# Performance work log

Measured on AMD Instinct MI355X. Metric: run time of the kernel, lower is better.

The kernel has to match this reference:

```python
import jax, jax.numpy as jnp
import numpy as np
import math

S, B, H, NH = 2048, 2, 2048, 16
HN = H // NH  # head dim = 128

def setup_inputs() -> dict:
    key = jax.random.key(0)
    ks = jax.random.split(key, 5)
    hidden_states = jax.random.normal(ks[0], (S, B, H), dtype=jnp.float32)
    # causal mask: True means masked (filled with -10000), broadcast over heads
    attention_mask = jnp.triu(jnp.ones((S, S), dtype=bool), k=1)[None, None].repeat(B, axis=0)
    w_qkv = jax.random.normal(ks[1], (3 * H, H), dtype=jnp.float32) * (1.0 / math.sqrt(H))
    b_qkv = jax.random.normal(ks[2], (3 * H,), dtype=jnp.float32) * 0.02
    w_dense = jax.random.normal(ks[3], (H, H), dtype=jnp.float32) * (1.0 / math.sqrt(H))
    b_dense = jax.random.normal(ks[4], (H,), dtype=jnp.float32) * 0.02
    return {"hidden_states": hidden_states, "attention_mask": attention_mask,
            "w_qkv": w_qkv, "b_qkv": b_qkv, "w_dense": w_dense, "b_dense": b_dense}

def reference(hidden_states, attention_mask, w_qkv, b_qkv, w_dense, b_dense):
    s, b, h = hidden_states.shape
    nh, hn = NH, h // NH
    # QKV projection (ColumnParallelLinear, world_size=1)
    qkv = hidden_states @ w_qkv.T + b_qkv                # [s, b, 3h]
    qkv = qkv.reshape(s, b, nh, 3 * hn)
    q, k, v = jnp.split(qkv, 3, axis=-1)                 # each [s, b, nh, hn]
    q = q.transpose(1, 2, 0, 3)                          # [b, nh, s, hn]
    k = k.transpose(1, 2, 0, 3)
    v = v.transpose(1, 2, 0, 3)
    # norm_factor = sqrt(hn)*coeff, softmax rescales by coeff -> net 1/sqrt(hn)
    scores = jnp.einsum('bnqh,bnkh->bnqk', q, k) / jnp.float32(math.sqrt(hn))
    scores = jnp.where(attention_mask, jnp.float32(-10000.0), scores)
    probs = jax.nn.softmax(scores, axis=-1)              # [b, nh, s, s]
    ctx = jnp.einsum('bnqk,bnkh->bnqh', probs, v)        # [b, nh, s, hn]
    ctx = ctx.transpose(2, 0, 1, 3).reshape(s, b, h)     # [s, b, h]
    # RowParallelLinear with skip_bias_add=True: bias returned separately
    output = ctx @ w_dense.T
    return output, b_dense
```

## Files before the change

kernel.cpp:

```cpp
#include <hip/hip_runtime.h>

typedef unsigned short u16;
typedef unsigned int   u32;
typedef __attribute__((ext_vector_type(8))) short bf16x8;
typedef __attribute__((ext_vector_type(4))) float f32x4;

#define S_LEN 2048
#define B_SZ  2
#define H_DIM 2048
#define NH_   16
#define HN_   128
#define M_TOK 4096
#define NQKV  6144
#define NT_   (S_LEN / 64)

#define BAR      asm volatile("s_barrier" ::: "memory")
#define WAITV(n) asm volatile("s_waitcnt vmcnt(" #n ")" ::: "memory")

__device__ __forceinline__ u16 f2bf(float f) {
    u32 x = __float_as_uint(f);
    return (u16)((x + 0x7fffu + ((x >> 16) & 1u)) >> 16);
}

__device__ __forceinline__ void async16(const void* g, void* l) {
    __builtin_amdgcn_global_load_lds((const __attribute__((address_space(1))) void*)g,
                                     (__attribute__((address_space(3))) void*)l,
                                     16, 0, 0);
}

__global__ __launch_bounds__(256) void cvt3(
    const float* __restrict__ a, u16* __restrict__ oa, int na,
    const float* __restrict__ b, u16* __restrict__ ob, int nb,
    const float* __restrict__ c, u16* __restrict__ oc, int nc)
{
    int g = blockIdx.x * 256 + threadIdx.x;
    const float* in; u16* out; int idx;
    if (g < na)           { in = a; out = oa; idx = g; }
    else if (g < na + nb) { in = b; out = ob; idx = g - na; }
    else if (g < na + nb + nc) { in = c; out = oc; idx = g - na - nb; }
    else return;
    int i = idx * 4;
    float4 v = *(const float4*)&in[i];
    ushort4 o;
    o.x = f2bf(v.x); o.y = f2bf(v.y); o.z = f2bf(v.z); o.w = f2bf(v.w);
    *(ushort4*)&out[i] = o;
}

template<int EPI, int MM, int NN>
__global__ __launch_bounds__(512, 2) void gemm8(
    const u16* __restrict__ A, const u16* __restrict__ W,
    const float* __restrict__ bias, float* __restrict__ Cout,
    u16* __restrict__ Qb, u16* __restrict__ Kb, u16* __restrict__ Vt)
{
    constexpr int K   = 2048;
    constexpr int NKT = K / 64;
    constexpr int NBN = NN / 256;
    constexpr int NWG = (MM / 256) * NBN;

    __shared__ __align__(16) u16 sA[2][256 * 64];
    __shared__ __align__(16) u16 sB[2][256 * 64];

    const int t = threadIdx.x, l = t & 63, w = t >> 6;
    const int quad = l >> 4, ln = l & 15;
    const int qw_r = w >> 2, qw_c = w & 3;

    int wg = blockIdx.x;
    wg = (wg & 7) * (NWG / 8) + (wg >> 3);
    const int m0 = (wg / NBN) * 256, n0 = (wg % NBN) * 256;

    const int srow = t >> 3;
    const int skc  = (t & 7) ^ (srow & 7);
    const u16* pA = A + (size_t)(m0 + srow) * K + skc * 8;
    const u16* pB = W + (size_t)(n0 + srow) * K + skc * 8;

#define STAGE_A(db, h, kt)                                                        \
    do {                                                                          \
        async16(pA + (size_t)(h) * 128 * K + (size_t)(kt) * 64,                   \
                &sA[db][(h) * 8192 + t * 8]);                                     \
        async16(pA + (size_t)(h) * 128 * K + (size_t)64 * K + (size_t)(kt) * 64,  \
                &sA[db][(h) * 8192 + t * 8 + 4096]);                              \
    } while (0)
#define STAGE_B(db, h, kt)                                                        \
    do {                                                                          \
        async16(pB + (size_t)(h) * 128 * K + (size_t)(kt) * 64,                   \
                &sB[db][(h) * 8192 + t * 8]);                                     \
        async16(pB + (size_t)(h) * 128 * K + (size_t)64 * K + (size_t)(kt) * 64,  \
                &sB[db][(h) * 8192 + t * 8 + 4096]);                              \
    } while (0)

    const int aBase = (qw_r * 64 + ln) * 64;
    const int bBase = (qw_c * 32 + ln) * 64;
    int swz[2];
#pragma unroll
    for (int ks = 0; ks < 2; ++ks)
        swz[ks] = ((ks * 4 + quad) ^ (ln & 7)) << 3;

    bf16x8 af[4][2];
    bf16x8 bS0[2][2];
    bf16x8 bS1[2][2];

#define RD_A(db, mq)                                                              \
    do {                                                                          \
        _Pragma("unroll") for (int mf = 0; mf < 4; ++mf)                          \
        _Pragma("unroll") for (int ks = 0; ks < 2; ++ks)                          \
            af[mf][ks] = *(const bf16x8*)&sA[db][aBase + (mq) * 8192 + mf * 1024  \
                                                + swz[ks]];                       \
    } while (0)
#define RD_B(db, nq, SET)                                                         \
    do {                                                                          \
        _Pragma("unroll") for (int nf = 0; nf < 2; ++nf)                          \
        _Pragma("unroll") for (int ks = 0; ks < 2; ++ks)                          \
            SET[nf][ks] = *(const bf16x8*)&sB[db][bBase + (nq) * 8192 + nf * 1024 \
                                                 + swz[ks]];                      \
    } while (0)

    f32x4 acc[4][4][2];
#pragma unroll
    for (int q = 0; q < 4; ++q)
#pragma unroll
        for (int mf = 0; mf < 4; ++mf)
#pragma unroll
            for (int nf = 0; nf < 2; ++nf)
#pragma unroll
                for (int r = 0; r < 4; ++r) acc[q][mf][nf][r] = 0.f;

#define MM16(q, SET)                                                              \
    do {                                                                          \
        __builtin_amdgcn_s_setprio(1);                                            \
        _Pragma("unroll") for (int mf = 0; mf < 4; ++mf)                          \
        _Pragma("unroll") for (int nf = 0; nf < 2; ++nf)                          \
        _Pragma("unroll") for (int ks = 0; ks < 2; ++ks)                          \
            acc[q][mf][nf] = __builtin_amdgcn_mfma_f32_16x16x32_bf16(             \
                af[mf][ks], SET[nf][ks], acc[q][mf][nf], 0, 0, 0);                \
        __builtin_amdgcn_s_setprio(0);                                            \
    } while (0)

    STAGE_A(0, 0, 0); STAGE_B(0, 0, 0); STAGE_B(0, 1, 0); STAGE_A(0, 1, 0);
    STAGE_A(1, 0, 1); STAGE_B(1, 0, 1); STAGE_B(1, 1, 1);
    WAITV(6);
    BAR;
    RD_A(0, 0); RD_B(0, 0, bS0);

#pragma unroll 1
    for (int i = 0; i < NKT / 2; ++i) {
        const int tt  = 2 * i;
        const int tp1 = tt + 1;
        const int tp2 = (tt + 2) & (NKT - 1);
        const int tp3 = (tt + 3) & (NKT - 1);

        STAGE_A(1, 1, tp1);
        MM16(0, bS0);
        RD_B(0, 1, bS1);
        BAR;
        STAGE_A(0, 0, tp2);
        MM16(1, bS1);
        RD_A(0, 1);
        BAR;
        STAGE_B(0, 0, tp2);
        MM16(3, bS1);
        WAITV(4);
        BAR;
        STAGE_B(0, 1, tp2);
        MM16(2, bS0);
        RD_A(1, 0); RD_B(1, 0, bS0);
        BAR;
        STAGE_A(0, 1, tp2);
        MM16(0, bS0);
        RD_B(1, 1, bS1);
        BAR;
        STAGE_A(1, 0, tp3);
        MM16(1, bS1);
        RD_A(1, 1);
        BAR;
        STAGE_B(1, 0, tp3);
        MM16(3, bS1);
        WAITV(4);
        BAR;
        STAGE_B(1, 1, tp3);
        MM16(2, bS0);
        RD_A(0, 0); RD_B(0, 0, bS0);
        BAR;
    }
#undef STAGE_A
#undef STAGE_B
#undef RD_A
#undef RD_B
#undef MM16

    if constexpr (EPI == 0) {
#pragma unroll
        for (int q = 0; q < 4; ++q) {
            const int mq = q >> 1, nq = q & 1;
#pragma unroll
            for (int mf = 0; mf < 4; ++mf)
#pragma unroll
                for (int nf = 0; nf < 2; ++nf) {
                    int col = n0 + nq * 128 + qw_c * 32 + nf * 16 + ln;
#pragma unroll
                    for (int r = 0; r < 4; ++r) {
                        int row = m0 + mq * 128 + qw_r * 64 + mf * 16 + quad * 4 + r;
                        Cout[(size_t)row * NN + col] = acc[q][mf][nf][r];
                    }
                }
        }
    } else {
        const float kQS = 0.08838834764831845f * 1.44269504088896340f;
#pragma unroll
        for (int q = 0; q < 4; ++q) {
            const int mq = q >> 1, nq = q & 1;
#pragma unroll
            for (int nf = 0; nf < 2; ++nf) {
                int col  = n0 + nq * 128 + qw_c * 32 + nf * 16 + ln;
                int head = col / 384;
                int g    = col - head * 384;
                int sec  = g >> 7;
                int d    = g & 127;
                float bv = bias[col];
#pragma unroll
                for (int mf = 0; mf < 4; ++mf)
#pragma unroll
                    for (int r = 0; r < 4; ++r) {
                        int tok = m0 + mq * 128 + qw_r * 64 + mf * 16 + quad * 4 + r;
                        int s = tok >> 1, bb = tok & 1;
                        float v = acc[q][mf][nf][r] + bv;
                        if (sec == 0)
                            Qb[((size_t)(bb * NH_ + head) * S_LEN + s) * HN_ + d] = f2bf(v * kQS);
                        else if (sec == 1)
                            Kb[((size_t)(bb * NH_ + head) * S_LEN + s) * HN_ + d] = f2bf(v);
                        else
                            Vt[((size_t)(bb * NH_ + head) * HN_ + d) * S_LEN + s] = f2bf(v);
                    }
            }
        }
    }
}

__global__ __launch_bounds__(256) void attn_mfma(
    const u16* __restrict__ Qb, const u16* __restrict__ Kb,
    const u16* __restrict__ Vt, u16* __restrict__ Ctx)
{
    __shared__ __align__(16) u16 Ks[2][16 * 64 * 8];
    __shared__ __align__(16) u16 Vs[2][16 * 64 * 8];
    __shared__ __align__(16) u16 Psm[4][16][72];

    const int t = threadIdx.x, l = t & 63, w = t >> 6;
    const int quad = l >> 4, ln = l & 15;
    const int j = blockIdx.x;
    const int n = blockIdx.y, b = blockIdx.z;
    const u16* Qh = Qb + (size_t)(b * NH_ + n) * S_LEN * HN_;
    const u16* Kh = Kb + (size_t)(b * NH_ + n) * S_LEN * HN_;
    const u16* Vh = Vt + (size_t)(b * NH_ + n) * HN_ * S_LEN;

#pragma unroll 1
    for (int phase = 0; phase < 2; ++phase) {
        const int qt = phase ? j : (NT_ - 1 - j);
        const int q0 = qt * 64;

#pragma unroll
        for (int i = 0; i < 4; ++i)
            async16(&Qh[(size_t)(q0 + i * 16 + ln) * HN_ + w * 32 + quad * 8],
                    &Ks[1][((i * 4 + w) * 64 + l) * 8]);
#pragma unroll
        for (int i = 0; i < 4; ++i) {
            async16(&Kh[(size_t)(i * 16 + ln) * HN_ + w * 32 + quad * 8],
                    &Ks[0][((i * 4 + w) * 64 + l) * 8]);
            int dv = i * 4 + w, dt = dv >> 1, ks = dv & 1;
            async16(&Vh[(size_t)(dt * 16 + ln) * S_LEN + ks * 32 + quad * 8],
                    &Vs[0][(dv * 64 + l) * 8]);
        }
        __syncthreads();

        bf16x8 qf[4];
#pragma unroll
        for (int ks = 0; ks < 4; ++ks)
            qf[ks] = *(const bf16x8*)&Ks[1][((w * 4 + ks) * 64 + l) * 8];
        __syncthreads();

        float m_i[4], l_i[4];
        f32x4 acco[8];
#pragma unroll
        for (int r = 0; r < 4; ++r) { m_i[r] = -1e30f; l_i[r] = 0.f; }
#pragma unroll
        for (int dt = 0; dt < 8; ++dt)
#pragma unroll
            for (int r = 0; r < 4; ++r) acco[dt][r] = 0.f;

#pragma unroll 1
        for (int kt = 0; kt <= qt; ++kt) {
            const int cur = kt & 1;

            if (kt < qt) {
                const int nxt = cur ^ 1;
#pragma unroll
                for (int i = 0; i < 4; ++i) {
                    async16(&Kh[(size_t)((kt + 1) * 64 + i * 16 + ln) * HN_ + w * 32 + quad * 8],
                            &Ks[nxt][((i * 4 + w) * 64 + l) * 8]);
                    int dv = i * 4 + w, dt = dv >> 1, ks = dv & 1;
                    async16(&Vh[(size_t)(dt * 16 + ln) * S_LEN + (kt + 1) * 64 + ks * 32 + quad * 8],
                            &Vs[nxt][(dv * 64 + l) * 8]);
                }
            }

            f32x4 sc[4];
#pragma unroll
            for (int nt = 0; nt < 4; ++nt)
#pragma unroll
                for (int r = 0; r < 4; ++r) sc[nt][r] = 0.f;
#pragma unroll
            for (int nt = 0; nt < 4; ++nt)
#pragma unroll
                for (int ks = 0; ks < 4; ++ks) {
                    bf16x8 kf = *(const bf16x8*)&Ks[cur][((nt * 4 + ks) * 64 + l) * 8];
                    sc[nt] = __builtin_amdgcn_mfma_f32_16x16x32_bf16(qf[ks], kf, sc[nt], 0, 0, 0);
                }

            if (kt == qt) {
#pragma unroll
                for (int nt = 0; nt < 4; ++nt)
#pragma unroll
                    for (int r = 0; r < 4; ++r)
                        if (nt * 16 + ln > w * 16 + quad * 4 + r) sc[nt][r] = -1e30f;
            }

            float corr[4];
#pragma unroll
            for (int r = 0; r < 4; ++r) {
                float mx = fmaxf(fmaxf(sc[0][r], sc[1][r]), fmaxf(sc[2][r], sc[3][r]));
                mx = fmaxf(mx, __shfl_xor(mx, 1));
                mx = fmaxf(mx, __shfl_xor(mx, 2));
                mx = fmaxf(mx, __shfl_xor(mx, 4));
                mx = fmaxf(mx, __shfl_xor(mx, 8));
                float mnew = fmaxf(m_i[r], mx);
                corr[r] = exp2f(m_i[r] - mnew);
                m_i[r] = mnew;
            }
#pragma unroll
            for (int r = 0; r < 4; ++r) {
                float ps = 0.f;
#pragma unroll
                for (int nt = 0; nt < 4; ++nt) {
                    float p = exp2f(sc[nt][r] - m_i[r]);
                    ps += p;
                    Psm[w][quad * 4 + r][nt * 16 + ln] = f2bf(p);
                }
                l_i[r] = l_i[r] * corr[r] + ps;
            }

#pragma unroll
            for (int dt = 0; dt < 8; ++dt)
#pragma unroll
                for (int r = 0; r < 4; ++r) acco[dt][r] *= corr[r];

            bf16x8 pf[2];
#pragma unroll
            for (int ks = 0; ks < 2; ++ks)
                pf[ks] = *(const bf16x8*)&Psm[w][ln][ks * 32 + quad * 8];
#pragma unroll
            for (int dt = 0; dt < 8; ++dt)
#pragma unroll
                for (int ks = 0; ks < 2; ++ks) {
                    bf16x8 vf = *(const bf16x8*)&Vs[cur][((dt * 2 + ks) * 64 + l) * 8];
                    acco[dt] = __builtin_amdgcn_mfma_f32_16x16x32_bf16(pf[ks], vf, acco[dt], 0, 0, 0);
                }
            __syncthreads();
        }

#pragma unroll
        for (int r = 0; r < 4; ++r) {
            float s = l_i[r];
            s += __shfl_xor(s, 1);
            s += __shfl_xor(s, 2);
            s += __shfl_xor(s, 4);
            s += __shfl_xor(s, 8);
            l_i[r] = 1.f / s;
        }
#pragma unroll
        for (int dt = 0; dt < 8; ++dt)
#pragma unroll
            for (int r = 0; r < 4; ++r) {
                int srow = q0 + w * 16 + quad * 4 + r;
                Ctx[((size_t)(srow * B_SZ + b)) * H_DIM + n * HN_ + dt * 16 + ln] =
                    f2bf(acco[dt][r] * l_i[r]);
            }
    }
}

__global__ void copy_bias(const float* __restrict__ b_dense, float* __restrict__ out)
{
    int t = blockIdx.x * 256 + threadIdx.x;
    if (t < H_DIM) out[(size_t)M_TOK * H_DIM + t] = b_dense[t];
}

extern "C" void kernel_launch(void* const* d_in, const int* in_sizes, int n_in,
                              void* d_out, int out_size, void* d_ws, size_t ws_size,
                              hipStream_t stream)
{
    const float* hs      = (const float*)d_in[0];
    const float* w_qkv   = (const float*)d_in[2];
    const float* b_qkv   = (const float*)d_in[3];
    const float* w_dense = (const float*)d_in[4];
    const float* b_dense = (const float*)d_in[5];
    float* out = (float*)d_out;

    u16* hs_bf = (u16*)d_ws;
    u16* wq_bf = hs_bf + (size_t)M_TOK * H_DIM;
    u16* wd_bf = wq_bf + (size_t)NQKV * H_DIM;
    u16* Qb    = wd_bf + (size_t)H_DIM * H_DIM;
    u16* Kb    = Qb    + (size_t)M_TOK * H_DIM;
    u16* Vt    = Kb    + (size_t)M_TOK * H_DIM;
    u16* Ctx   = Vt    + (size_t)M_TOK * H_DIM;

    const int g1 = (M_TOK * H_DIM) / 4;
    const int g2 = (NQKV * H_DIM) / 4;
    const int g3 = (H_DIM * H_DIM) / 4;
    cvt3<<<(g1 + g2 + g3 + 255) / 256, 256, 0, stream>>>(
        hs, hs_bf, g1, w_qkv, wq_bf, g2, w_dense, wd_bf, g3);

    gemm8<1, M_TOK, NQKV><<<(M_TOK / 256) * (NQKV / 256), 512, 0, stream>>>(
        hs_bf, wq_bf, b_qkv, nullptr, Qb, Kb, Vt);

    attn_mfma<<<dim3(NT_ / 2, NH_, B_SZ), 256, 0, stream>>>(Qb, Kb, Vt, Ctx);

    gemm8<0, M_TOK, H_DIM><<<(M_TOK / 256) * (H_DIM / 256), 512, 0, stream>>>(
        Ctx, wd_bf, nullptr, out, nullptr, nullptr, nullptr);

    copy_bias<<<(H_DIM + 255) / 256, 256, 0, stream>>>(b_dense, out);
}
```

Baseline: 427.9 us.

## Double attention query tile to 128 rows and restructure K/V staging

The attention kernel now handles 128 query rows per block (32 per wave, two MFMA row fragments), so each K/V tile loaded into LDS feeds twice as many rows. Q fragments are loaded straight from global memory into registers. K stays double-buffered while V becomes single-buffered and is refilled after the PV product, with explicit vmcnt waits and lgkm barriers instead of __syncthreads. The P scratch buffer uses an XOR swizzle to avoid LDS bank conflicts. This halves the grid to 256 blocks and raises register pressure, which may reduce occupancy and parallelism.

```diff
diff --git a/kernel.cpp b/kernel.cpp
--- a/kernel.cpp
+++ b/kernel.cpp
@@ -12,10 +12,10 @@
 #define HN_   128
 #define M_TOK 4096
 #define NQKV  6144
-#define NT_   (S_LEN / 64)
 
 #define BAR      asm volatile("s_barrier" ::: "memory")
 #define WAITV(n) asm volatile("s_waitcnt vmcnt(" #n ")" ::: "memory")
+#define LGKM_BAR asm volatile("s_waitcnt lgkmcnt(0)\n\ts_barrier" ::: "memory")
 
 __device__ __forceinline__ u16 f2bf(float f) {
     u32 x = __float_as_uint(f);
@@ -235,13 +235,13 @@
     }
 }
 
-__global__ __launch_bounds__(256) void attn_mfma(
+__global__ __launch_bounds__(256, 2) void attn_mfma(
     const u16* __restrict__ Qb, const u16* __restrict__ Kb,
     const u16* __restrict__ Vt, u16* __restrict__ Ctx)
 {
     __shared__ __align__(16) u16 Ks[2][16 * 64 * 8];
-    __shared__ __align__(16) u16 Vs[2][16 * 64 * 8];
-    __shared__ __align__(16) u16 Psm[4][16][72];
+    __shared__ __align__(16) u16 Vs[16 * 64 * 8];
+    __shared__ __align__(16) u16 Psm[4 * 32 * 64];
 
     const int t = threadIdx.x, l = t & 63, w = t >> 6;
     const int quad = l >> 4, ln = l & 15;
@@ -250,139 +250,179 @@
     const u16* Qh = Qb + (size_t)(b * NH_ + n) * S_LEN * HN_;
     const u16* Kh = Kb + (size_t)(b * NH_ + n) * S_LEN * HN_;
     const u16* Vh = Vt + (size_t)(b * NH_ + n) * HN_ * S_LEN;
+    u16* Pw = &Psm[w * 2048];
+
+#define STAGE_K(buf, kt)                                                           \
+    do { _Pragma("unroll") for (int i = 0; i < 4; ++i)                             \
+        async16(&Kh[(size_t)((kt) * 64 + i * 16 + ln) * HN_ + w * 32 + quad * 8],  \
+                &Ks[buf][((i * 4 + w) * 64 + l) * 8]); } while (0)
+#define STAGE_V(kt)                                                               \
+    do { _Pragma("unroll") for (int i = 0; i < 4; ++i) {                          \
+        int dv = i * 4 + w, dvt = dv >> 1, ks = dv & 1;                           \
+        async16(&Vh[(size_t)(dvt * 16 + ln) * S_LEN + (kt) * 64 + ks * 32 + quad * 8], \
+                &Vs[(dv * 64 + l) * 8]); } } while (0)
 
 #pragma unroll 1
     for (int phase = 0; phase < 2; ++phase) {
-        const int qt = phase ? j : (NT_ - 1 - j);
-        const int q0 = qt * 64;
-
-#pragma unroll
-        for (int i = 0; i < 4; ++i)
-            async16(&Qh[(size_t)(q0 + i * 16 + ln) * HN_ + w * 32 + quad * 8],
-                    &Ks[1][((i * 4 + w) * 64 + l) * 8]);
-#pragma unroll
-        for (int i = 0; i < 4; ++i) {
-            async16(&Kh[(size_t)(i * 16 + ln) * HN_ + w * 32 + quad * 8],
-                    &Ks[0][((i * 4 + w) * 64 + l) * 8]);
-            int dv = i * 4 + w, dt = dv >> 1, ks = dv & 1;
-            async16(&Vh[(size_t)(dt * 16 + ln) * S_LEN + ks * 32 + quad * 8],
-                    &Vs[0][(dv * 64 + l) * 8]);
-        }
-        __syncthreads();
-
-        bf16x8 qf[4];
-#pragma unroll
-        for (int ks = 0; ks < 4; ++ks)
-            qf[ks] = *(const bf16x8*)&Ks[1][((w * 4 + ks) * 64 + l) * 8];
-        __syncthreads();
-
-        float m_i[4], l_i[4];
-        f32x4 acco[8];
-#pragma unroll
-        for (int r = 0; r < 4; ++r) { m_i[r] = -1e30f; l_i[r] = 0.f; }
-#pragma unroll
-        for (int dt = 0; dt < 8; ++dt)
-#pragma unroll
-            for (int r = 0; r < 4; ++r) acco[dt][r] = 0.f;
+        const int qt  = phase ? j : (15 - j);
+        const int q0  = qt * 128;
+        const int nkt = 2 * qt + 2;
+
+        bf16x8 qf[2][4];
+#pragma unroll
+        for (int mf = 0; mf < 2; ++mf)
+#pragma unroll
+            for (int ks = 0; ks < 4; ++ks)
+                qf[mf][ks] = *(const bf16x8*)
+                    &Qh[(size_t)(q0 + w * 32 + mf * 16 + ln) * HN_ + ks * 32 + quad * 8];
+
+        LGKM_BAR;
+        STAGE_K(0, 0);
+        STAGE_V(0);
+
+        float m_i[2][4], l_i[2][4];
+        f32x4 acco[2][8];
+#pragma unroll
+        for (int mf = 0; mf < 2; ++mf)
+#pragma unroll
+            for (int r = 0; r < 4; ++r) { m_i[mf][r] = -1e30f; l_i[mf][r] = 0.f; }
+#pragma unroll
+        for (int mf = 0; mf < 2; ++mf)
+#pragma unroll
+            for (int dt = 0; dt < 8; ++dt)
+#pragma unroll
+                for (int r = 0; r < 4; ++r) acco[mf][dt][r] = 0.f;
 
 #pragma unroll 1
-        for (int kt = 0; kt <= qt; ++kt) {
+        for (int kt = 0; kt < nkt; ++kt) {
             const int cur = kt & 1;
-
-            if (kt < qt) {
-                const int nxt = cur ^ 1;
-#pragma unroll
-                for (int i = 0; i < 4; ++i) {
-                    async16(&Kh[(size_t)((kt + 1) * 64 + i * 16 + ln) * HN_ + w * 32 + quad * 8],
-                            &Ks[nxt][((i * 4 + w) * 64 + l) * 8]);
-                    int dv = i * 4 + w, dt = dv >> 1, ks = dv & 1;
-                    async16(&Vh[(size_t)(dt * 16 + ln) * S_LEN + (kt + 1) * 64 + ks * 32 + quad * 8],
-                            &Vs[nxt][(dv * 64 + l) * 8]);
-                }
-            }
-
-            f32x4 sc[4];
-#pragma unroll
-            for (int nt = 0; nt < 4; ++nt)
-#pragma unroll
-                for (int r = 0; r < 4; ++r) sc[nt][r] = 0.f;
+            const bool last = (kt == nkt - 1);
+
+            WAITV(4);
+            LGKM_BAR;
+            if (!last) STAGE_K(cur ^ 1, kt + 1);
+
+            f32x4 sc[2][4];
+#pragma unroll
+            for (int mf = 0; mf < 2; ++mf)
+#pragma unroll
+                for (int nt = 0; nt < 4; ++nt)
+#pragma unroll
+                    for (int r = 0; r < 4; ++r) sc[mf][nt][r] = 0.f;
 #pragma unroll
             for (int nt = 0; nt < 4; ++nt)
 #pragma unroll
                 for (int ks = 0; ks < 4; ++ks) {
                     bf16x8 kf = *(const bf16x8*)&Ks[cur][((nt * 4 + ks) * 64 + l) * 8];
-                    sc[nt] = __builtin_amdgcn_mfma_f32_16x16x32_bf16(qf[ks], kf, sc[nt], 0, 0, 0);
-                }
-
-            if (kt == qt) {
-#pragma unroll
-                for (int nt = 0; nt < 4; ++nt)
-#pragma unroll
-                    for (int r = 0; r < 4; ++r)
-                        if (nt * 16 + ln > w * 16 + quad * 4 + r) sc[nt][r] = -1e30f;
+#pragma unroll
+                    for (int mf = 0; mf < 2; ++mf)
+                        sc[mf][nt] = __builtin_amdgcn_mfma_f32_16x16x32_bf16(
+                            qf[mf][ks], kf, sc[mf][nt], 0, 0, 0);
+                }
+
+            if (kt >= 2 * qt) {
+#pragma unroll
+                for (int mf = 0; mf < 2; ++mf)
+#pragma unroll
+                    for (int nt = 0; nt < 4; ++nt)
+#pragma unroll
+                        for (int r = 0; r < 4; ++r)
+                            if ((kt - 2 * qt) * 64 + nt * 16 + ln >
+                                w * 32 + mf * 16 + quad * 4 + r)
+                                sc[mf][nt][r] = -1e30f;
             }
 
-            float corr[4];
+            float corr[2][4];
+#pragma unroll
+            for (int mf = 0; mf < 2; ++mf)
+#pragma unroll
+                for (int r = 0; r < 4; ++r) {
+                    float mx = fmaxf(fmaxf(sc[mf][0][r], sc[mf][1][r]),
+                                     fmaxf(sc[mf][2][r], sc[mf][3][r]));
+                    mx = fmaxf(mx, __shfl_xor(mx, 1));
+                    mx = fmaxf(mx, __shfl_xor(mx, 2));
+                    mx = fmaxf(mx, __shfl_xor(mx, 4));
+                    mx = fmaxf(mx, __shfl_xor(mx, 8));
+                    float mnew = fmaxf(m_i[mf][r], mx);
+                    corr[mf][r] = exp2f(m_i[mf][r] - mnew);
+                    m_i[mf][r] = mnew;
+                }
+#pragma unroll
+            for (int mf = 0; mf < 2; ++mf)
+#pragma unroll
+                for (int r = 0; r < 4; ++r) {
+                    float ps = 0.f;
+                    const int row = mf * 16 + quad * 4 + r;
+                    const int sw = (row ^ (row >> 3)) & 7;
+#pragma unroll
+                    for (int nt = 0; nt < 4; ++nt) {
+                        float p = exp2f(sc[mf][nt][r] - m_i[mf][r]);
+                        ps += p;
+                        Pw[row * 64 + (((nt * 2 + (ln >> 3)) ^ sw) << 3) + (ln & 7)] = f2bf(p);
+                    }
+                    l_i[mf][r] = l_i[mf][r] * corr[mf][r] + ps;
+                }
+#pragma unroll
+            for (int mf = 0; mf < 2; ++mf)
+#pragma unroll
+                for (int dt = 0; dt < 8; ++dt)
+#pragma unroll
+                    for (int r = 0; r < 4; ++r) acco[mf][dt][r] *= corr[mf][r];
+
+            if (!last) { WAITV(4); } else { WAITV(0); }
+            LGKM_BAR;
+
+            bf16x8 pf[2][2];
+#pragma unroll
+            for (int mf = 0; mf < 2; ++mf)
+#pragma unroll
+                for (int ks = 0; ks < 2; ++ks) {
+                    const int row = mf * 16 + ln;
+                    const int sw = (row ^ (row >> 3)) & 7;
+                    pf[mf][ks] = *(const bf16x8*)
+                        &Pw[row * 64 + (((ks * 4 + quad) ^ sw) << 3)];
+                }
+#pragma unroll
+            for (int dt = 0; dt < 8; ++dt)
+#pragma unroll
+                for (int ks = 0; ks < 2; ++ks) {
+                    bf16x8 vf = *(const bf16x8*)&Vs[((dt * 2 + ks) * 64 + l) * 8];
+#pragma unroll
+                    for (int mf = 0; mf < 2; ++mf)
+                        acco[mf][dt] = __builtin_amdgcn_mfma_f32_16x16x32_bf16(
+                            pf[mf][ks], vf, acco[mf][dt], 0, 0, 0);
+                }
+
+            if (!last) {
+                LGKM_BAR;
+                STAGE_V(kt + 1);
+            }
+        }
+
+#pragma unroll
+        for (int mf = 0; mf < 2; ++mf)
 #pragma unroll
             for (int r = 0; r < 4; ++r) {
-                float mx = fmaxf(fmaxf(sc[0][r], sc[1][r]), fmaxf(sc[2][r], sc[3][r]));
-                mx = fmaxf(mx, __shfl_xor(mx, 1));
-                mx = fmaxf(mx, __shfl_xor(mx, 2));
-                mx = fmaxf(mx, __shfl_xor(mx, 4));
-                mx = fmaxf(mx, __shfl_xor(mx, 8));
-                float mnew = fmaxf(m_i[r], mx);
-                corr[r] = exp2f(m_i[r] - mnew);
-                m_i[r] = mnew;
+                float s = l_i[mf][r];
+                s += __shfl_xor(s, 1);
+                s += __shfl_xor(s, 2);
+                s += __shfl_xor(s, 4);
+                s += __shfl_xor(s, 8);
+                l_i[mf][r] = 1.f / s;
             }
 #pragma unroll
-            for (int r = 0; r < 4; ++r) {
-                float ps = 0.f;
-#pragma unroll
-                for (int nt = 0; nt < 4; ++nt) {
-                    float p = exp2f(sc[nt][r] - m_i[r]);
-                    ps += p;
-                    Psm[w][quad * 4 + r][nt * 16 + ln] = f2bf(p);
-                }
-                l_i[r] = l_i[r] * corr[r] + ps;
-            }
-
+        for (int mf = 0; mf < 2; ++mf)
 #pragma unroll
             for (int dt = 0; dt < 8; ++dt)
 #pragma unroll
-                for (int r = 0; r < 4; ++r) acco[dt][r] *= corr[r];
-
-            bf16x8 pf[2];
-#pragma unroll
-            for (int ks = 0; ks < 2; ++ks)
-                pf[ks] = *(const bf16x8*)&Psm[w][ln][ks * 32 + quad * 8];
-#pragma unroll
-            for (int dt = 0; dt < 8; ++dt)
-#pragma unroll
-                for (int ks = 0; ks < 2; ++ks) {
-                    bf16x8 vf = *(const bf16x8*)&Vs[cur][((dt * 2 + ks) * 64 + l) * 8];
-                    acco[dt] = __builtin_amdgcn_mfma_f32_16x16x32_bf16(pf[ks], vf, acco[dt], 0, 0, 0);
-                }
-            __syncthreads();
-        }
-
-#pragma unroll
-        for (int r = 0; r < 4; ++r) {
-            float s = l_i[r];
-            s += __shfl_xor(s, 1);
-            s += __shfl_xor(s, 2);
-            s += __shfl_xor(s, 4);
-            s += __shfl_xor(s, 8);
-            l_i[r] = 1.f / s;
-        }
-#pragma unroll
-        for (int dt = 0; dt < 8; ++dt)
-#pragma unroll
-            for (int r = 0; r < 4; ++r) {
-                int srow = q0 + w * 16 + quad * 4 + r;
-                Ctx[((size_t)(srow * B_SZ + b)) * H_DIM + n * HN_ + dt * 16 + ln] =
-                    f2bf(acco[dt][r] * l_i[r]);
-            }
+                for (int r = 0; r < 4; ++r) {
+                    int srow = q0 + w * 32 + mf * 16 + quad * 4 + r;
+                    Ctx[((size_t)(srow * B_SZ + b)) * H_DIM + n * HN_ + dt * 16 + ln] =
+                        f2bf(acco[mf][dt][r] * l_i[mf][r]);
+                }
     }
+#undef STAGE_K
+#undef STAGE_V
 }
 
 __global__ void copy_bias(const float* __restrict__ b_dense, float* __restrict__ out)
@@ -419,7 +459,7 @@
     gemm8<1, M_TOK, NQKV><<<(M_TOK / 256) * (NQKV / 256), 512, 0, stream>>>(
         hs_bf, wq_bf, b_qkv, nullptr, Qb, Kb, Vt);
 
-    attn_mfma<<<dim3(NT_ / 2, NH_, B_SZ), 256, 0, stream>>>(Qb, Kb, Vt, Ctx);
+    attn_mfma<<<dim3(8, NH_, B_SZ), 256, 0, stream>>>(Qb, Kb, Vt, Ctx);
 
     gemm8<0, M_TOK, H_DIM><<<(M_TOK / 256) * (H_DIM / 256), 512, 0, stream>>>(
         Ctx, wd_bf, nullptr, out, nullptr, nullptr, nullptr);
```

After: 492.9 us. 15.2% more time.
